# Performance work log

Hardware: AMD Instinct MI355X
Metric: run time of the kernel (lower is better)

Reference implementation:

```python
import jax, jax.numpy as jnp
import numpy as np

B, T, D = 2, 2048, 1024
NH, NKV, HD, RD = 16, 4, 64, 32


def apply_rope(x, cos, sin):
    # x: [B, H, T, hd]; cos/sin: [T, 1, 1, RD//2]
    r = cos.shape[-1] * 2
    x1 = x[..., : r // 2]
    x2 = x[..., r // 2 : r]
    x_pass = x[..., r:]
    c = cos.reshape(1, 1, cos.shape[0], -1)  # [1,1,T,RD//2]
    s = sin.reshape(1, 1, sin.shape[0], -1)
    return jnp.concatenate([x1 * c - x2 * s, x1 * s + x2 * c, x_pass], axis=-1)


def setup_inputs() -> dict:
    key = jax.random.key(0)
    ks = jax.random.split(key, 8)
    # realistic partial-RoPE angle tables
    inv_freq = 1.0 / (10000.0 ** (np.arange(0, RD, 2, dtype=np.float32) / RD))
    ang = np.arange(T, dtype=np.float32)[:, None] * inv_freq[None, :]  # [T, RD//2]
    cos = jnp.asarray(np.cos(ang)).reshape(T, 1, 1, RD // 2)
    sin = jnp.asarray(np.sin(ang)).reshape(T, 1, 1, RD // 2)
    return {
        "x": jax.random.normal(ks[0], (B, T, D), dtype=jnp.float32),
        "cos": cos,
        "sin": sin,
        "v0": jax.random.normal(ks[1], (B, NH, T, HD), dtype=jnp.float32),
        "Wqkv": jax.random.normal(ks[2], ((NH + 2 * NKV) * HD, D), dtype=jnp.float32) * (D ** -0.5),
        "Wproj": jax.random.normal(ks[3], (D, D), dtype=jnp.float32) * (D ** -0.5),
        "vrl_alpha": jnp.full((NH,), 0.1, dtype=jnp.float32),
        "qk_scale": 0.5 + jax.random.uniform(ks[4], (NH,), dtype=jnp.float32),
    }


def reference(x, cos, sin, v0, Wqkv, Wproj, vrl_alpha, qk_scale):
    nH, nKV, hd = NH, NKV, HD
    qkv = jnp.einsum("btd,ed->bte", x, Wqkv)  # [B,T,(nH+2nKV)*hd]
    q = qkv[..., : nH * hd].reshape(B, T, nH, hd).transpose(0, 2, 1, 3)
    k = qkv[..., nH * hd : (nH + nKV) * hd].reshape(B, T, nKV, hd).transpose(0, 2, 1, 3)
    v = qkv[..., (nH + nKV) * hd :].reshape(B, T, nKV, hd).transpose(0, 2, 1, 3)
    q = apply_rope(q, cos, sin)
    k = apply_rope(k, cos, sin)
    reps = nH // nKV
    k_exp = jnp.repeat(k, reps, axis=1)  # [B,nH,T,hd]
    v_exp = jnp.repeat(v, reps, axis=1)
    # VRL blend (layer_idx > 0)
    alpha = jax.nn.sigmoid(vrl_alpha)[None, :, None, None]
    v_exp = (1.0 - alpha) * v_exp + alpha * v0
    # per-head learned qk scale, split as sqrt on q and k
    sfac = jnp.sqrt(qk_scale[None, :, None, None] * (hd ** -0.5))
    q_s = q * sfac
    k_s = k_exp * sfac
    # causal SDPA (default scale 1/sqrt(hd))
    scores = jnp.einsum("bhqd,bhkd->bhqk", q_s, k_s) * (hd ** -0.5)
    causal = jnp.tril(jnp.ones((T, T), dtype=bool))
    scores = jnp.where(causal[None, None], scores, jnp.float32(-1e30))
    attn = jax.nn.softmax(scores, axis=-1)
    y = jnp.einsum("bhqk,bhkd->bhqd", attn, v_exp)
    y = y.transpose(0, 2, 1, 3).reshape(B, T, D)
    out = jnp.einsum("btd,ed->bte", y, Wproj)
    return out, v0
```

## Files before the change

kernel.cpp:

```cpp
#include <hip/hip_runtime.h>
#include <hip/hip_bf16.h>

#define B_   2
#define T_   2048
#define D_   1024
#define NH_  16
#define NKV_ 4
#define HD_  64
#define E_   1536
#define LOG2E 1.4426950408889634f

typedef __attribute__((ext_vector_type(8))) __bf16 bf16x8;
typedef __attribute__((ext_vector_type(4))) __bf16 bf16x4;
typedef __attribute__((ext_vector_type(4))) float f32x4;

static __device__ __forceinline__ void gld_lds16(const unsigned short* g, unsigned short* l) {
  __builtin_amdgcn_global_load_lds(
      (const __attribute__((address_space(1))) unsigned int*)(unsigned long long)(const void*)g,
      (__attribute__((address_space(3))) unsigned int*)(unsigned int)(unsigned long long)(void*)l,
      16, 0, 0);
}

static __device__ __forceinline__ float fexp2(float x) {
  float r; asm("v_exp_f32 %0, %1" : "=v"(r) : "v"(x)); return r;
}
static __device__ __forceinline__ float fmax3(float a, float b, float c) {
  float r; asm("v_max3_f32 %0, %1, %2, %3" : "=v"(r) : "v"(a), "v"(b), "v"(c)); return r;
}
static __device__ __forceinline__ float frcp(float x) {
  float r; asm("v_rcp_f32 %0, %1" : "=v"(r) : "v"(x)); return r;
}

#define PIPE_BARRIER(N) {                                   \
  asm volatile("s_waitcnt vmcnt(" #N ")" ::: "memory");     \
  __builtin_amdgcn_s_barrier();                             \
  __builtin_amdgcn_sched_barrier(0); }

#define CVT8(dst, f0, f1) {                                                    \
  dst[0] = (__bf16)f0.x; dst[1] = (__bf16)f0.y;                               \
  dst[2] = (__bf16)f0.z; dst[3] = (__bf16)f0.w;                               \
  dst[4] = (__bf16)f1.x; dst[5] = (__bf16)f1.y;                               \
  dst[6] = (__bf16)f1.z; dst[7] = (__bf16)f1.w; }

__global__ void k_convert_all(const float* __restrict__ x, const float* __restrict__ wq,
                              const float* __restrict__ wp,
                              unsigned short* __restrict__ xb, unsigned short* __restrict__ wqb,
                              unsigned short* __restrict__ wpb) {
  int i = blockIdx.x * blockDim.x + threadIdx.x;
  const float* src; unsigned short* dst; int j;
  if (i < 524288)      { src = x;  dst = xb;  j = i; }
  else if (i < 720896) { src = wq; dst = wqb; j = i - 524288; }
  else                 { src = wp; dst = wpb; j = i - 720896; }
  int n = j >> 7, c8 = (j & 127) * 8;
  const float4* p = (const float4*)(src + (size_t)n * 1024 + c8);
  float4 a = p[0], b = p[1];
  bf16x8 o; CVT8(o, a, b);
  *(bf16x8*)(dst + (size_t)n * 1024 + (c8 ^ ((n & 7) * 8))) = o;
}

__global__ __launch_bounds__(256) void k_gemm_qkv(
    const unsigned short* __restrict__ A,
    const unsigned short* __restrict__ W,
    const float* __restrict__ cosT, const float* __restrict__ sinT,
    const float* __restrict__ v0,
    const float* __restrict__ vrl, const float* __restrict__ qks,
    unsigned short* __restrict__ qb, unsigned short* __restrict__ kb,
    unsigned short* __restrict__ vb) {
  __shared__ __align__(16) unsigned short As[2][128 * 64];
  __shared__ __align__(16) unsigned short Ws[2][128 * 64];
  int tid = threadIdx.x;
  int w = tid >> 6, l = tid & 63, lo = l & 15, hi = l >> 4;
  int wm = w >> 1, wn = w & 1;
  int f = blockIdx.y * 12 + blockIdx.x;
  int f2 = (f & 7) * 48 + (f >> 3);
  int bn = f2 % 12, bm = f2 / 12;
  int rsw = (lo & 7) * 8;

  const unsigned short* Ab = A + (size_t)bm * 128 * 1024;
  const unsigned short* Wb = W + (size_t)bn * 128 * 1024;

  f32x4 acc[4][4];
#pragma unroll
  for (int mi = 0; mi < 4; ++mi)
#pragma unroll
    for (int ni = 0; ni < 4; ++ni) acc[mi][ni] = (f32x4){0.f, 0.f, 0.f, 0.f};

#define STAGE(kt, buf) {                                                       \
  int k0 = (kt) * 64;                                                         \
  _Pragma("unroll") for (int ii = 0; ii < 4; ++ii) {                          \
    int sb = ii * 256 + tid;                                                  \
    gld_lds16(Ab + (size_t)(sb >> 3) * 1024 + k0 + (sb & 7) * 8,              \
              &As[buf][(sb & ~63) * 8]);                                      \
  }                                                                           \
  _Pragma("unroll") for (int ii = 0; ii < 4; ++ii) {                          \
    int sb = ii * 256 + tid;                                                  \
    gld_lds16(Wb + (size_t)(sb >> 3) * 1024 + k0 + (sb & 7) * 8,              \
              &Ws[buf][(sb & ~63) * 8]);                                      \
  } }

  STAGE(0, 0);
  __syncthreads();

  for (int kt = 0; kt < 16; ++kt) {
    int cur = kt & 1;
    bool pf = (kt + 1) < 16;
    if (pf) STAGE(kt + 1, cur ^ 1);
    __builtin_amdgcn_s_setprio(1);
#pragma unroll
    for (int kk = 0; kk < 2; ++kk) {
      int c0 = (kk * 32 + hi * 8) ^ rsw;
      bf16x8 af[4], wf[4];
#pragma unroll
      for (int mi = 0; mi < 4; ++mi)
        af[mi] = *(const bf16x8*)&As[cur][(wm * 64 + mi * 16 + lo) * 64 + c0];
#pragma unroll
      for (int ni = 0; ni < 4; ++ni)
        wf[ni] = *(const bf16x8*)&Ws[cur][(wn * 64 + ni * 16 + lo) * 64 + c0];
#pragma unroll
      for (int mi = 0; mi < 4; ++mi)
#pragma unroll
        for (int ni = 0; ni < 4; ++ni)
          acc[mi][ni] = __builtin_amdgcn_mfma_f32_16x16x32_bf16(af[mi], wf[ni], acc[mi][ni], 0, 0, 0);
    }
    __builtin_amdgcn_s_setprio(0);
    __syncthreads();
  }
#undef STAGE

  int hg = bn * 2 + wn;
  if (hg < 20) {
    int isq = (hg < 16);
    int h = isq ? hg : hg - 16;
    float sc = isq ? (qks[h] * (LOG2E / 64.0f)) : 1.0f;
    unsigned short* base = isq ? qb : kb;
    int nheads = isq ? NH_ : NKV_;
#pragma unroll
    for (int mi = 0; mi < 4; ++mi) {
#pragma unroll
      for (int r = 0; r < 4; ++r) {
        int row = bm * 128 + wm * 64 + mi * 16 + hi * 4 + r;
        int b = row >> 11, t = row & 2047;
        float c = cosT[t * 16 + lo], s = sinT[t * 16 + lo];
        float a0 = acc[mi][0][r], a1 = acc[mi][1][r];
        __bf16* dp = (__bf16*)(base + ((size_t)(b * nheads + h) * T_ + t) * 64);
        int ts = isq ? 0 : (8 * (t & 7));
        dp[lo ^ ts]        = (__bf16)((a0 * c - a1 * s) * sc);
        dp[(16 + lo) ^ ts] = (__bf16)((a0 * s + a1 * c) * sc);
        dp[(32 + lo) ^ ts] = (__bf16)(acc[mi][2][r] * sc);
        dp[(48 + lo) ^ ts] = (__bf16)(acc[mi][3][r] * sc);
      }
    }
  } else {
    int hv = hg - 20;
    float av[4];
#pragma unroll
    for (int j = 0; j < 4; ++j) av[j] = 1.0f / (1.0f + __expf(-vrl[hv * 4 + j]));
#pragma unroll
    for (int mi = 0; mi < 4; ++mi) {
      int t0g = bm * 128 + wm * 64 + mi * 16 + hi * 4;
      int b = t0g >> 11, t0 = t0g & 2047;
#pragma unroll
      for (int ni = 0; ni < 4; ++ni) {
        int d = ni * 16 + lo;
#pragma unroll
        for (int j = 0; j < 4; ++j) {
          float a = av[j], na = 1.0f - a;
          const float* v0p = v0 + ((size_t)(b * NH_ + hv * 4 + j) * T_ + t0) * 64 + d;
          bf16x4 vv;
#pragma unroll
          for (int r = 0; r < 4; ++r)
            vv[r] = (__bf16)(na * acc[mi][ni][r] + a * v0p[(size_t)r * 64]);
          *(bf16x4*)((unsigned short*)vb + ((size_t)(b * NH_ + hv * 4 + j) * 64 + d) * T_ +
                     (t0 ^ (8 * (lo & 7)))) = vv;
        }
      }
    }
  }
}

__global__ __launch_bounds__(256) void k_gemm_proj(
    const unsigned short* __restrict__ A,
    const unsigned short* __restrict__ W,
    const float* __restrict__ v0,
    float* __restrict__ C, float* __restrict__ out2) {
  __shared__ __align__(16) unsigned short As[2][128 * 64];
  __shared__ __align__(16) unsigned short Ws[2][128 * 64];
  int tid = threadIdx.x;

  if (blockIdx.y >= 32) {
    int idx = ((blockIdx.y - 32) * 8 + blockIdx.x) * 256 + tid;
    const float4* src = (const float4*)v0;
    float4* dst = (float4*)out2;
#pragma unroll
    for (int i = 0; i < 32; ++i) dst[idx + i * 32768] = src[idx + i * 32768];
    return;
  }

  int w = tid >> 6, l = tid & 63, lo = l & 15, hi = l >> 4;
  int wm = w >> 1, wn = w & 1;
  int f = blockIdx.y * 8 + blockIdx.x;
  int f2 = (f & 7) * 32 + (f >> 3);
  int bn = f2 & 7, bm = f2 >> 3;
  int rsw = (lo & 7) * 8;

  const unsigned short* Ab = A + (size_t)bm * 128 * 1024;
  const unsigned short* Wb = W + (size_t)bn * 128 * 1024;

  f32x4 acc[4][4];
#pragma unroll
  for (int mi = 0; mi < 4; ++mi)
#pragma unroll
    for (int ni = 0; ni < 4; ++ni) acc[mi][ni] = (f32x4){0.f, 0.f, 0.f, 0.f};

#define STAGE(kt, buf) {                                                       \
  int k0 = (kt) * 64;                                                         \
  _Pragma("unroll") for (int ii = 0; ii < 4; ++ii) {                          \
    int sb = ii * 256 + tid;                                                  \
    gld_lds16(Ab + (size_t)(sb >> 3) * 1024 + k0 + (sb & 7) * 8,              \
              &As[buf][(sb & ~63) * 8]);                                      \
  }                                                                           \
  _Pragma("unroll") for (int ii = 0; ii < 4; ++ii) {                          \
    int sb = ii * 256 + tid;                                                  \
    gld_lds16(Wb + (size_t)(sb >> 3) * 1024 + k0 + (sb & 7) * 8,              \
              &Ws[buf][(sb & ~63) * 8]);                                      \
  } }

  STAGE(0, 0);
  __syncthreads();
  for (int kt = 0; kt < 16; ++kt) {
    int cur = kt & 1;
    bool pf = (kt + 1) < 16;
    if (pf) STAGE(kt + 1, cur ^ 1);
    __builtin_amdgcn_s_setprio(1);
#pragma unroll
    for (int kk = 0; kk < 2; ++kk) {
      int c0 = (kk * 32 + hi * 8) ^ rsw;
      bf16x8 af[4], wf[4];
#pragma unroll
      for (int mi = 0; mi < 4; ++mi)
        af[mi] = *(const bf16x8*)&As[cur][(wm * 64 + mi * 16 + lo) * 64 + c0];
#pragma unroll
      for (int ni = 0; ni < 4; ++ni)
        wf[ni] = *(const bf16x8*)&Ws[cur][(wn * 64 + ni * 16 + lo) * 64 + c0];
#pragma unroll
      for (int mi = 0; mi < 4; ++mi)
#pragma unroll
        for (int ni = 0; ni < 4; ++ni)
          acc[mi][ni] = __builtin_amdgcn_mfma_f32_16x16x32_bf16(af[mi], wf[ni], acc[mi][ni], 0, 0, 0);
    }
    __builtin_amdgcn_s_setprio(0);
    __syncthreads();
  }
#undef STAGE

#pragma unroll
  for (int mi = 0; mi < 4; ++mi) {
#pragma unroll
    for (int r = 0; r < 4; ++r) {
      int row = bm * 128 + wm * 64 + mi * 16 + hi * 4 + r;
      float* cp = C + (size_t)row * D_ + bn * 128 + wn * 64 + lo;
#pragma unroll
      for (int ni = 0; ni < 4; ++ni) cp[ni * 16] = acc[mi][ni][r];
    }
  }
}

static __device__ __forceinline__ void stage_kv8(const unsigned short* Kb, const unsigned short* Vb,
                                                 int kv0, int w, int l,
                                                 unsigned short* KsB, unsigned short* VsB) {
  gld_lds16(Kb + (size_t)kv0 * 64 + w * 512 + l * 8, KsB + w * 512);
  gld_lds16(Vb + (size_t)(w * 8 + (l >> 3)) * T_ + kv0 + (l & 7) * 8, VsB + w * 512);
}

__device__ __forceinline__ void softmax_state(f32x4 (&s)[4], float& m, float& lsum,
                                              f32x4 (&y)[4], unsigned short* PsW,
                                              int lo, int hi, int swz) {
  float a0 = fmax3(s[0][0], s[0][1], s[0][2]);
  float a1 = fmax3(s[0][3], s[1][0], s[1][1]);
  float a2 = fmax3(s[1][2], s[1][3], s[2][0]);
  float a3 = fmax3(s[2][1], s[2][2], s[2][3]);
  float a4 = fmax3(s[3][0], s[3][1], s[3][2]);
  float pm = fmaxf(fmax3(a0, a1, a2), fmax3(a3, a4, s[3][3]));
  if (!__all(pm <= m + 8.0f)) {
    pm = fmaxf(pm, __shfl_xor(pm, 16));
    pm = fmaxf(pm, __shfl_xor(pm, 32));
    float mnew = fmaxf(m, pm);
    float sc = fexp2(m - mnew);
    lsum *= sc;
#pragma unroll
    for (int r = 0; r < 4; ++r) {
      float scr = __shfl(sc, hi * 4 + r);
#pragma unroll
      for (int nf = 0; nf < 4; ++nf) y[nf][r] *= scr;
    }
    m = mnew;
  }
  float rs = 0.f;
#pragma unroll
  for (int nt = 0; nt < 4; ++nt) {
    float p0 = fexp2(s[nt][0] - m);
    float p1 = fexp2(s[nt][1] - m);
    float p2 = fexp2(s[nt][2] - m);
    float p3 = fexp2(s[nt][3] - m);
    rs += (p0 + p1) + (p2 + p3);
    bf16x4 pk;
    pk[0] = (__bf16)p0; pk[1] = (__bf16)p1; pk[2] = (__bf16)p2; pk[3] = (__bf16)p3;
    *(bf16x4*)(PsW + lo * 64 + ((nt * 16 + hi * 4) ^ swz)) = pk;
  }
  lsum += rs;
}

__global__ __launch_bounds__(512, 2) void k_attn(const unsigned short* __restrict__ Q,
                                                 const unsigned short* __restrict__ Kp,
                                                 const unsigned short* __restrict__ Vtp,
                                                 unsigned short* __restrict__ Y) {
  int p = blockIdx.y, h = blockIdx.x, b = blockIdx.z;
  if (b == 1) p = 15 - p;
  int tid = threadIdx.x;
  int w = tid >> 6, l = tid & 63, lo = l & 15, hi = l >> 4;
  int kh = h >> 2;
  int qtA = p, qtB = 31 - p;
  int ntB = qtB + 1;
  int st = w >> 2, wq = w & 3;
  int qt = st ? qtA : qtB;
  int q0 = qt * 64 + wq * 16;
  int swz = 8 * (lo & 7);

  __shared__ __align__(16) unsigned short Ks[3][4096];
  __shared__ __align__(16) unsigned short Vs[3][4096];
  __shared__ __align__(16) unsigned short Ps[8192];
  unsigned short* PsW = &Ps[w * 1024];

  const unsigned short* Qb = Q + ((size_t)(b * NH_ + h) * T_) * 64;
  const unsigned short* Kb = Kp + ((size_t)(b * NKV_ + kh) * T_) * 64;
  const unsigned short* Vb = Vtp + ((size_t)(b * NH_ + h) * 64) * T_;

  bf16x8 q_0 = *(const bf16x8*)(Qb + (size_t)(q0 + lo) * 64 + hi * 8);
  bf16x8 q_1 = *(const bf16x8*)(Qb + (size_t)(q0 + lo) * 64 + 32 + hi * 8);

  f32x4 y[4];
#pragma unroll
  for (int nf = 0; nf < 4; ++nf) y[nf] = (f32x4){0.f, 0.f, 0.f, 0.f};
  float m = -INFINITY, lsum = 0.f;

  stage_kv8(Kb, Vb, 0, w, l, Ks[0], Vs[0]);
  stage_kv8(Kb, Vb, 64, w, l, Ks[1], Vs[1]);
  int cur = 0, wbuf = 2;

  for (int kt = 0; kt < ntB; ++kt) {
    if (kt + 1 < ntB) PIPE_BARRIER(2) else PIPE_BARRIER(0);
    if (kt + 2 < ntB) stage_kv8(Kb, Vb, (kt + 2) * 64, w, l, Ks[wbuf], Vs[wbuf]);

    if (kt <= qt) {
      int kv0 = kt * 64;
      const unsigned short* KsC = Ks[cur];
      const unsigned short* VsC = Vs[cur];

      f32x4 s[4];
      __builtin_amdgcn_s_setprio(1);
#pragma unroll
      for (int nt = 0; nt < 4; ++nt) {
        int rrow = (nt * 16 + lo) * 64;
        int c0 = (hi * 8) ^ swz;
        bf16x8 kf0 = *(const bf16x8*)&KsC[rrow + c0];
        bf16x8 kf1 = *(const bf16x8*)&KsC[rrow + (c0 ^ 32)];
        f32x4 a = (f32x4){0.f, 0.f, 0.f, 0.f};
        a = __builtin_amdgcn_mfma_f32_16x16x32_bf16(kf0, q_0, a, 0, 0, 0);
        a = __builtin_amdgcn_mfma_f32_16x16x32_bf16(kf1, q_1, a, 0, 0, 0);
        s[nt] = a;
      }
      __builtin_amdgcn_s_setprio(0);

      if (kt == qt) {
#pragma unroll
        for (int nt = 0; nt < 4; ++nt)
#pragma unroll
          for (int r = 0; r < 4; ++r)
            if (kv0 + nt * 16 + hi * 4 + r > q0 + lo) s[nt][r] = -1e30f;
      }

      softmax_state(s, m, lsum, y, PsW, lo, hi, swz);

      __builtin_amdgcn_s_setprio(1);
#pragma unroll
      for (int kc = 0; kc < 2; ++kc) {
        int pcol = (kc * 32 + hi * 8) ^ swz;
        bf16x8 pa = *(const bf16x8*)&PsW[lo * 64 + pcol];
#pragma unroll
        for (int nf = 0; nf < 4; ++nf) {
          bf16x8 vf = *(const bf16x8*)&VsC[(nf * 16 + lo) * 64 + pcol];
          y[nf] = __builtin_amdgcn_mfma_f32_16x16x32_bf16(pa, vf, y[nf], 0, 0, 0);
        }
      }
      __builtin_amdgcn_s_setprio(0);
    }

    cur = (cur == 2) ? 0 : cur + 1;
    wbuf = (wbuf == 2) ? 0 : wbuf + 1;
  }

  lsum += __shfl_xor(lsum, 16);
  lsum += __shfl_xor(lsum, 32);
  float inv = frcp(lsum);
#pragma unroll
  for (int r = 0; r < 4; ++r) {
    float iv = __shfl(inv, hi * 4 + r);
    int t = q0 + hi * 4 + r;
    int sw = 8 * (t & 7);
    __bf16* yp = (__bf16*)(Y + ((size_t)(b * T_ + t)) * D_ + h * 64);
#pragma unroll
    for (int nf = 0; nf < 4; ++nf)
      yp[(nf * 16 + lo) ^ sw] = (__bf16)(y[nf][r] * iv);
  }
}

extern "C" void kernel_launch(void* const* d_in, const int* in_sizes, int n_in,
                              void* d_out, int out_size, void* d_ws, size_t ws_size,
                              hipStream_t stream) {
  const float* x     = (const float*)d_in[0];
  const float* cosT  = (const float*)d_in[1];
  const float* sinT  = (const float*)d_in[2];
  const float* v0    = (const float*)d_in[3];
  const float* Wqkv  = (const float*)d_in[4];
  const float* Wproj = (const float*)d_in[5];
  const float* vrl   = (const float*)d_in[6];
  const float* qks   = (const float*)d_in[7];
  float* out = (float*)d_out;

  char* ws = (char*)d_ws;
  unsigned short* xb     = (unsigned short*)ws;
  unsigned short* wqkvb  = (unsigned short*)(ws + 8388608);
  unsigned short* wprojb = (unsigned short*)(ws + 11534336);
  unsigned short* qb     = (unsigned short*)(ws + 13631488);
  unsigned short* kb     = (unsigned short*)(ws + 22020096);
  unsigned short* vb     = (unsigned short*)(ws + 24117248);
  unsigned short* yb     = (unsigned short*)(ws + 32505856);

  k_convert_all<<<3328, 256, 0, stream>>>(x, Wqkv, Wproj, xb, wqkvb, wprojb);

  k_gemm_qkv<<<dim3(12, 32), 256, 0, stream>>>(xb, wqkvb, cosT, sinT, v0, vrl, qks, qb, kb, vb);

  k_attn<<<dim3(NH_, 16, B_), 512, 0, stream>>>(qb, kb, vb, yb);

  k_gemm_proj<<<dim3(8, 48), 256, 0, stream>>>(yb, wprojb, v0, out, out + 4194304);
}
```

Measured before the change: 91.69 us.

## Switch attention to 32x32 MFMA with split-key warps and LDS merge

Rewrites the attention inner loop to use 32x32x16 bf16 MFMA instead of 16x16x32. Each warp now owns 32 queries and half of every 64-key tile, so pairs of warps split the keys. Their partial softmax states and outputs are combined at the end through shared memory. This cuts LDS fragment loads and cross-lane shuffles per FLOP and skips one masked quarter on diagonal tiles, at the cost of an extra merge pass, more registers and two extra block barriers.

```diff
diff --git a/kernel.cpp b/kernel.cpp
--- a/kernel.cpp
+++ b/kernel.cpp
@@ -13,6 +13,7 @@
 typedef __attribute__((ext_vector_type(8))) __bf16 bf16x8;
 typedef __attribute__((ext_vector_type(4))) __bf16 bf16x4;
 typedef __attribute__((ext_vector_type(4))) float f32x4;
+typedef __attribute__((ext_vector_type(16))) float f32x16;
 
 static __device__ __forceinline__ void gld_lds16(const unsigned short* g, unsigned short* l) {
   __builtin_amdgcn_global_load_lds(
@@ -272,44 +273,6 @@
   gld_lds16(Vb + (size_t)(w * 8 + (l >> 3)) * T_ + kv0 + (l & 7) * 8, VsB + w * 512);
 }
 
-__device__ __forceinline__ void softmax_state(f32x4 (&s)[4], float& m, float& lsum,
-                                              f32x4 (&y)[4], unsigned short* PsW,
-                                              int lo, int hi, int swz) {
-  float a0 = fmax3(s[0][0], s[0][1], s[0][2]);
-  float a1 = fmax3(s[0][3], s[1][0], s[1][1]);
-  float a2 = fmax3(s[1][2], s[1][3], s[2][0]);
-  float a3 = fmax3(s[2][1], s[2][2], s[2][3]);
-  float a4 = fmax3(s[3][0], s[3][1], s[3][2]);
-  float pm = fmaxf(fmax3(a0, a1, a2), fmax3(a3, a4, s[3][3]));
-  if (!__all(pm <= m + 8.0f)) {
-    pm = fmaxf(pm, __shfl_xor(pm, 16));
-    pm = fmaxf(pm, __shfl_xor(pm, 32));
-    float mnew = fmaxf(m, pm);
-    float sc = fexp2(m - mnew);
-    lsum *= sc;
-#pragma unroll
-    for (int r = 0; r < 4; ++r) {
-      float scr = __shfl(sc, hi * 4 + r);
-#pragma unroll
-      for (int nf = 0; nf < 4; ++nf) y[nf][r] *= scr;
-    }
-    m = mnew;
-  }
-  float rs = 0.f;
-#pragma unroll
-  for (int nt = 0; nt < 4; ++nt) {
-    float p0 = fexp2(s[nt][0] - m);
-    float p1 = fexp2(s[nt][1] - m);
-    float p2 = fexp2(s[nt][2] - m);
-    float p3 = fexp2(s[nt][3] - m);
-    rs += (p0 + p1) + (p2 + p3);
-    bf16x4 pk;
-    pk[0] = (__bf16)p0; pk[1] = (__bf16)p1; pk[2] = (__bf16)p2; pk[3] = (__bf16)p3;
-    *(bf16x4*)(PsW + lo * 64 + ((nt * 16 + hi * 4) ^ swz)) = pk;
-  }
-  lsum += rs;
-}
-
 __global__ __launch_bounds__(512, 2) void k_attn(const unsigned short* __restrict__ Q,
                                                  const unsigned short* __restrict__ Kp,
                                                  const unsigned short* __restrict__ Vtp,
@@ -317,80 +280,112 @@
   int p = blockIdx.y, h = blockIdx.x, b = blockIdx.z;
   if (b == 1) p = 15 - p;
   int tid = threadIdx.x;
-  int w = tid >> 6, l = tid & 63, lo = l & 15, hi = l >> 4;
-  int kh = h >> 2;
+  int w = tid >> 6, l = tid & 63;
+  int l31 = l & 31, lh = l >> 5;
+  int kh = w & 1, wq = (w >> 1) & 1, st = w >> 2;
+  int kha = kh * 32;
   int qtA = p, qtB = 31 - p;
   int ntB = qtB + 1;
-  int st = w >> 2, wq = w & 3;
   int qt = st ? qtA : qtB;
-  int q0 = qt * 64 + wq * 16;
-  int swz = 8 * (lo & 7);
-
-  __shared__ __align__(16) unsigned short Ks[3][4096];
-  __shared__ __align__(16) unsigned short Vs[3][4096];
-  __shared__ __align__(16) unsigned short Ps[8192];
-  unsigned short* PsW = &Ps[w * 1024];
+  int q0w = qt * 64 + wq * 32;
+
+  __shared__ __align__(16) unsigned short SMEM[32768];
+  unsigned short* Kbase = SMEM;
+  unsigned short* Vbase = SMEM + 3 * 4096;
+  unsigned short* PsW   = SMEM + 6 * 4096 + w * 1024 + l31 * 32;
 
   const unsigned short* Qb = Q + ((size_t)(b * NH_ + h) * T_) * 64;
-  const unsigned short* Kb = Kp + ((size_t)(b * NKV_ + kh) * T_) * 64;
+  const unsigned short* Kb = Kp + ((size_t)(b * NKV_ + (h >> 2)) * T_) * 64;
   const unsigned short* Vb = Vtp + ((size_t)(b * NH_ + h) * 64) * T_;
 
-  bf16x8 q_0 = *(const bf16x8*)(Qb + (size_t)(q0 + lo) * 64 + hi * 8);
-  bf16x8 q_1 = *(const bf16x8*)(Qb + (size_t)(q0 + lo) * 64 + 32 + hi * 8);
-
-  f32x4 y[4];
-#pragma unroll
-  for (int nf = 0; nf < 4; ++nf) y[nf] = (f32x4){0.f, 0.f, 0.f, 0.f};
+  bf16x8 qf[4];
+#pragma unroll
+  for (int ds = 0; ds < 4; ++ds)
+    qf[ds] = *(const bf16x8*)(Qb + (size_t)(q0w + l31) * 64 + ds * 16 + lh * 8);
+
+  int key = kha + l31;
+  int kbase = key * 64, ksw = 8 * (key & 7);
+  int vb0 = l31 * 64, vsw = 8 * (l31 & 7);
+  int vb1 = (32 + l31) * 64;
+  int psw = 8 * (l31 & 3);
+
+  f32x16 y0{}, y1{};
   float m = -INFINITY, lsum = 0.f;
 
-  stage_kv8(Kb, Vb, 0, w, l, Ks[0], Vs[0]);
-  stage_kv8(Kb, Vb, 64, w, l, Ks[1], Vs[1]);
+  stage_kv8(Kb, Vb, 0, w, l, Kbase, Vbase);
+  stage_kv8(Kb, Vb, 64, w, l, Kbase + 4096, Vbase + 4096);
   int cur = 0, wbuf = 2;
 
   for (int kt = 0; kt < ntB; ++kt) {
     if (kt + 1 < ntB) PIPE_BARRIER(2) else PIPE_BARRIER(0);
-    if (kt + 2 < ntB) stage_kv8(Kb, Vb, (kt + 2) * 64, w, l, Ks[wbuf], Vs[wbuf]);
-
-    if (kt <= qt) {
+    if (kt + 2 < ntB) stage_kv8(Kb, Vb, (kt + 2) * 64, w, l, Kbase + wbuf * 4096, Vbase + wbuf * 4096);
+
+    bool act = (kt < qt) || (kt == qt && !(kh == 1 && wq == 0));
+    if (act) {
       int kv0 = kt * 64;
-      const unsigned short* KsC = Ks[cur];
-      const unsigned short* VsC = Vs[cur];
-
-      f32x4 s[4];
+      const unsigned short* KsC = Kbase + cur * 4096;
+      const unsigned short* VsC = Vbase + cur * 4096;
+
+      f32x16 s{};
       __builtin_amdgcn_s_setprio(1);
 #pragma unroll
-      for (int nt = 0; nt < 4; ++nt) {
-        int rrow = (nt * 16 + lo) * 64;
-        int c0 = (hi * 8) ^ swz;
-        bf16x8 kf0 = *(const bf16x8*)&KsC[rrow + c0];
-        bf16x8 kf1 = *(const bf16x8*)&KsC[rrow + (c0 ^ 32)];
-        f32x4 a = (f32x4){0.f, 0.f, 0.f, 0.f};
-        a = __builtin_amdgcn_mfma_f32_16x16x32_bf16(kf0, q_0, a, 0, 0, 0);
-        a = __builtin_amdgcn_mfma_f32_16x16x32_bf16(kf1, q_1, a, 0, 0, 0);
-        s[nt] = a;
+      for (int ds = 0; ds < 4; ++ds) {
+        bf16x8 kf = *(const bf16x8*)&KsC[kbase + ((ds * 16 + lh * 8) ^ ksw)];
+        s = __builtin_amdgcn_mfma_f32_32x32x16_bf16(kf, qf[ds], s, 0, 0, 0);
       }
       __builtin_amdgcn_s_setprio(0);
 
       if (kt == qt) {
-#pragma unroll
-        for (int nt = 0; nt < 4; ++nt)
-#pragma unroll
-          for (int r = 0; r < 4; ++r)
-            if (kv0 + nt * 16 + hi * 4 + r > q0 + lo) s[nt][r] = -1e30f;
-      }
-
-      softmax_state(s, m, lsum, y, PsW, lo, hi, swz);
+        int qg = q0w + l31;
+#pragma unroll
+        for (int i = 0; i < 16; ++i) {
+          int keyg = kv0 + kha + (i & 3) + 8 * (i >> 2) + 4 * lh;
+          if (keyg > qg) s[i] = -1e30f;
+        }
+      }
+
+      float pm = fmax3(s[0], s[1], s[2]);
+      pm = fmax3(pm, s[3], s[4]);
+      pm = fmax3(pm, s[5], s[6]);
+      pm = fmax3(pm, s[7], s[8]);
+      pm = fmax3(pm, s[9], s[10]);
+      pm = fmax3(pm, s[11], s[12]);
+      pm = fmax3(pm, s[13], s[14]);
+      pm = fmaxf(pm, s[15]);
+      pm = fmaxf(pm, __shfl_xor(pm, 32));
+      if (!__all(pm <= m + 8.0f)) {
+        float mnew = fmaxf(m, pm);
+        float sc = fexp2(m - mnew);
+        lsum *= sc;
+#pragma unroll
+        for (int i = 0; i < 16; ++i) { y0[i] *= sc; y1[i] *= sc; }
+        m = mnew;
+      }
+      float rs = 0.f;
+#pragma unroll
+      for (int i = 0; i < 16; ++i) {
+        float pv = fexp2(s[i] - m);
+        s[i] = pv;
+        rs += pv;
+      }
+      lsum += rs;
+
+#pragma unroll
+      for (int g = 0; g < 4; ++g) {
+        bf16x4 pk;
+        pk[0] = (__bf16)s[g * 4 + 0]; pk[1] = (__bf16)s[g * 4 + 1];
+        pk[2] = (__bf16)s[g * 4 + 2]; pk[3] = (__bf16)s[g * 4 + 3];
+        *(bf16x4*)(PsW + ((8 * g + 4 * lh) ^ psw)) = pk;
+      }
 
       __builtin_amdgcn_s_setprio(1);
 #pragma unroll
-      for (int kc = 0; kc < 2; ++kc) {
-        int pcol = (kc * 32 + hi * 8) ^ swz;
-        bf16x8 pa = *(const bf16x8*)&PsW[lo * 64 + pcol];
-#pragma unroll
-        for (int nf = 0; nf < 4; ++nf) {
-          bf16x8 vf = *(const bf16x8*)&VsC[(nf * 16 + lo) * 64 + pcol];
-          y[nf] = __builtin_amdgcn_mfma_f32_16x16x32_bf16(pa, vf, y[nf], 0, 0, 0);
-        }
+      for (int kw = 0; kw < 2; ++kw) {
+        bf16x8 pb = *(const bf16x8*)(PsW + ((kw * 16 + lh * 8) ^ psw));
+        bf16x8 va0 = *(const bf16x8*)&VsC[vb0 + ((kha + kw * 16 + lh * 8) ^ vsw)];
+        y0 = __builtin_amdgcn_mfma_f32_32x32x16_bf16(va0, pb, y0, 0, 0, 0);
+        bf16x8 va1 = *(const bf16x8*)&VsC[vb1 + ((kha + kw * 16 + lh * 8) ^ vsw)];
+        y1 = __builtin_amdgcn_mfma_f32_32x32x16_bf16(va1, pb, y1, 0, 0, 0);
       }
       __builtin_amdgcn_s_setprio(0);
     }
@@ -399,18 +394,40 @@
     wbuf = (wbuf == 2) ? 0 : wbuf + 1;
   }
 
-  lsum += __shfl_xor(lsum, 16);
-  lsum += __shfl_xor(lsum, 32);
-  float inv = frcp(lsum);
-#pragma unroll
-  for (int r = 0; r < 4; ++r) {
-    float iv = __shfl(inv, hi * 4 + r);
-    int t = q0 + hi * 4 + r;
+  __syncthreads();
+  float lt = lsum + __shfl_xor(lsum, 32);
+  float* buf = (float*)SMEM;
+  int slot = ((st * 2 + wq) * 64 + l) * 36;
+  if (kh) {
+#pragma unroll
+    for (int i = 0; i < 16; ++i) { buf[slot + i] = y0[i]; buf[slot + 16 + i] = y1[i]; }
+    buf[slot + 32] = m;
+    buf[slot + 33] = lt;
+  }
+  __syncthreads();
+  if (!kh) {
+    float m1 = buf[slot + 32], l1 = buf[slot + 33];
+    float M = fmaxf(m, m1);
+    float f0 = fexp2(m - M), f1 = fexp2(m1 - M);
+    float inv = frcp(lt * f0 + l1 * f1);
+    int t = q0w + l31;
     int sw = 8 * (t & 7);
     __bf16* yp = (__bf16*)(Y + ((size_t)(b * T_ + t)) * D_ + h * 64);
 #pragma unroll
-    for (int nf = 0; nf < 4; ++nf)
-      yp[(nf * 16 + lo) ^ sw] = (__bf16)(y[nf][r] * iv);
+    for (int dB = 0; dB < 2; ++dB) {
+#pragma unroll
+      for (int g = 0; g < 4; ++g) {
+        int dbase = dB * 32 + g * 8 + 4 * lh;
+        bf16x4 o;
+#pragma unroll
+        for (int r = 0; r < 4; ++r) {
+          float self = dB ? y1[g * 4 + r] : y0[g * 4 + r];
+          float other = buf[slot + dB * 16 + g * 4 + r];
+          o[r] = (__bf16)((self * f0 + other * f1) * inv);
+        }
+        *(bf16x4*)(yp + (dbase ^ sw)) = o;
+      }
+    }
   }
 }
 
```

Result: slower. 97.45 us (+6.3%).
